# Optimization experiments

Measured on AMD Instinct MI355X. Metric: run time of the kernel, lower is better.

The kernel has to match this reference:

```python
import jax, jax.numpy as jnp
from jax import lax
import numpy as np

DN = ('NCHW', 'OIHW', 'NCHW')
PAD = [(1, 1), (1, 1)]  # padding=1 each side
STRIDE = (1, 1)


def setup_inputs() -> dict:
    key = jax.random.key(0)
    k0, k1, k2, k3, k4, k5 = jax.random.split(key, 6)
    B, Cin, Cout, H, W, K, FES = 32, 96, 144, 56, 56, 3, 3
    fan_main = Cin * K * K
    fan_extra = FES * K * K
    x = jax.random.normal(k0, (B, Cin, H, W), dtype=jnp.float32)
    extra_inputs = jax.random.normal(k1, (B, Cout * FES), dtype=jnp.float32)
    Wm = jax.random.normal(k2, (Cout, Cin, K, K), dtype=jnp.float32) / np.sqrt(fan_main)
    bm = jax.random.normal(k3, (Cout,), dtype=jnp.float32) * 0.01
    Wx = jax.random.normal(k4, (Cout, FES, K, K), dtype=jnp.float32) / np.sqrt(fan_extra)
    bx = jax.random.normal(k5, (Cout,), dtype=jnp.float32) * 0.01
    return {"x": x, "extra_inputs": extra_inputs, "Wm": Wm, "bm": bm, "Wx": Wx, "bx": bx}


def reference(x, extra_inputs, Wm, bm, Wx, bx):
    # main path: standard conv + bias
    main = lax.conv_general_dilated(x, Wm, STRIDE, PAD, dimension_numbers=DN)
    main = main + bm[None, :, None, None]

    B = x.shape[0]
    Cout, FES, kh, kw = Wx.shape
    H2, W2 = main.shape[2], main.shape[3]

    # Extra path: each extra conv operates on a spatially-constant map, so
    # conv(const_c) = const_c * conv(ones). Compute per-(out,fes)-kernel response
    # to a ones map once (captures zero-padding boundary effects exactly),
    # then combine via a batched einsum — collapsing the per-channel loop.
    ones = jnp.ones((1, 1, x.shape[2], x.shape[3]), dtype=x.dtype)
    M = lax.conv_general_dilated(
        ones, Wx.reshape(Cout * FES, 1, kh, kw), STRIDE, PAD, dimension_numbers=DN
    )  # [1, Cout*FES, H2, W2]
    M = M.reshape(Cout, FES, H2, W2)

    extra = extra_inputs.reshape(B, Cout, FES)
    extra_out = jnp.einsum('bif,ifhw->bihw', extra, M) + bx[None, :, None, None]

    return main + extra_out
```

## Files before the change

kernel.cpp:

```cpp
#include <hip/hip_runtime.h>
#include <hip/hip_bf16.h>

#define B_    32
#define CIN   96
#define COUT  144
#define H_    56
#define W_    56
#define HW    3136
#define NPIX  100352
#define KTOT  864
#define MT    128
#define TAPSZ (COUT*CIN)
#define W2    58
#define PLANE (W2*W2)
#define XTP_SHORTS ((size_t)B_ * PLANE * CIN)

typedef short  short8  __attribute__((ext_vector_type(8)));
typedef float  floatx4 __attribute__((ext_vector_type(4)));

__device__ __forceinline__ unsigned short f2bf(float f) {
    union { float f; unsigned int u; } v; v.f = f;
    unsigned int u = v.u;
    return (unsigned short)((u + 0x7FFFu + ((u >> 16) & 1u)) >> 16);
}

__device__ __forceinline__ void glds16(const void* g, void* l) {
    __builtin_amdgcn_global_load_lds(
        (const __attribute__((address_space(1))) unsigned int*)g,
        (__attribute__((address_space(3))) unsigned int*)l, 16, 0, 0);
}

#define TB 1568
#define WB 486
#define EB 18
#define ZB 342
__global__ __launch_bounds__(256) void prep_all(const float* __restrict__ x,
                                                unsigned short* __restrict__ xTp,
                                                const float* __restrict__ Wm,
                                                unsigned short* __restrict__ Wt,
                                                const float* __restrict__ extra,
                                                const float* __restrict__ Wx,
                                                const float* __restrict__ bm,
                                                const float* __restrict__ bx,
                                                float* __restrict__ E) {
    __shared__ __align__(16) unsigned short tile[64][CIN + 8];
    int blk = blockIdx.x;
    int t = threadIdx.x;
    if (blk < TB) {
        int b   = blk / 49;
        int hw0 = (blk % 49) * 64;
        const float* xb = x + (size_t)b * CIN * HW;
        for (int i = t; i < CIN * 16; i += 256) {
            int ci = i >> 4, seg = i & 15;
            float4 v = *(const float4*)(xb + (size_t)ci * HW + hw0 + seg * 4);
            int hwl = seg * 4;
            tile[hwl + 0][ci] = f2bf(v.x);
            tile[hwl + 1][ci] = f2bf(v.y);
            tile[hwl + 2][ci] = f2bf(v.z);
            tile[hwl + 3][ci] = f2bf(v.w);
        }
        __syncthreads();
        int row = t >> 2, part = t & 3;
        int hw = hw0 + row;
        int h  = hw / W_;
        int w  = hw - h * W_;
        const uint4* s = (const uint4*)&tile[row][part * 24];
        uint4* d = (uint4*)(xTp + ((size_t)((b * W2 + h + 1) * W2 + (w + 1))) * CIN
                                + part * 24);
        d[0] = s[0]; d[1] = s[1]; d[2] = s[2];
    } else if (blk < TB + WB) {
        int i = (blk - TB) * 256 + t;
        int tap = i / 13824;
        int r1  = i - tap * 13824;
        int g   = r1 / 1152;
        int r2  = r1 - g * 1152;
        int co  = r2 >> 3;
        int e   = r2 & 7;
        int ci  = g * 8 + e;
        Wt[i] = f2bf(Wm[((size_t)co * CIN + ci) * 9 + tap]);
    } else if (blk < TB + WB + EB) {
        int i = (blk - TB - WB) * 256 + t;
        int b = i / COUT, co = i - b * COUT;
        float base = bm[co] + bx[co];
        float m[3][3] = {{0,0,0},{0,0,0},{0,0,0}};
        for (int f = 0; f < 3; ++f) {
            float e = extra[(size_t)b * (COUT * 3) + co * 3 + f];
            const float* w = Wx + ((size_t)co * 3 + f) * 9;
            for (int rc = 0; rc < 3; ++rc) {
                int kh0 = (rc == 0) ? 1 : 0;
                int kh1 = (rc == 2) ? 1 : 2;
                for (int cc = 0; cc < 3; ++cc) {
                    int kw0 = (cc == 0) ? 1 : 0;
                    int kw1 = (cc == 2) ? 1 : 2;
                    float s = 0.f;
                    for (int kh = kh0; kh <= kh1; ++kh)
                        for (int kw = kw0; kw <= kw1; ++kw)
                            s += w[kh * 3 + kw];
                    m[rc][cc] += e * s;
                }
            }
        }
        float* dst = E + (size_t)i * 9;
        for (int rc = 0; rc < 3; ++rc)
            for (int cc = 0; cc < 3; ++cc)
                dst[rc * 3 + cc] = base + m[rc][cc];
    } else {
        int i = (blk - TB - WB - EB) * 256 + t;
        int b = i / 2736;
        int r = i - b * 2736;
        size_t base_b = (size_t)b * PLANE * CIN;
        size_t addr;
        if (r < 696) {
            addr = base_b + (size_t)r * 8;
        } else if (r < 1392) {
            addr = base_b + (size_t)57 * W2 * CIN + (size_t)(r - 696) * 8;
        } else if (r < 2064) {
            int r2 = r - 1392;
            int h = 1 + r2 / 12, u = r2 - (r2 / 12) * 12;
            addr = base_b + (size_t)(h * W2) * CIN + (size_t)u * 8;
        } else {
            int r2 = r - 2064;
            int h = 1 + r2 / 12, u = r2 - (r2 / 12) * 12;
            addr = base_b + (size_t)(h * W2 + 57) * CIN + (size_t)u * 8;
        }
        *(short8*)(xTp + addr) = (short8){0, 0, 0, 0, 0, 0, 0, 0};
    }
}

#define MFMA16(A, B, C) __builtin_amdgcn_mfma_f32_16x16x32_bf16(A, B, C, 0, 0, 0)

__global__ __launch_bounds__(256, 3) void conv_gemm(const unsigned short* __restrict__ xTp,
                                                    const unsigned short* __restrict__ Wt,
                                                    const float* __restrict__ E,
                                                    float* __restrict__ out) {
    __shared__ __align__(16) unsigned short Bs[TAPSZ];

    int tid = threadIdx.x;
    int wv = tid >> 6, lane = tid & 63;
    int r16 = lane & 15, q = lane >> 4;
    int pixBase = blockIdx.x * MT;

    floatx4 acc[2][9];
    #pragma unroll
    for (int m = 0; m < 2; ++m)
        #pragma unroll
        for (int n = 0; n < 9; ++n)
            acc[m][n] = (floatx4){0.f, 0.f, 0.f, 0.f};

    int aOff[2];
    #pragma unroll
    for (int ms = 0; ms < 2; ++ms) {
        int p = pixBase + wv * 32 + ms * 16 + r16;
        int b = p / HW;
        int hw = p - b * HW;
        int h = hw / W_;
        int w = hw - h * W_;
        aOff[ms] = ((b * W2 + h + 1) * W2 + (w + 1)) * CIN + q * 8;
    }

    const bool bTail = (tid < 192);

    const unsigned short* BpBase = Bs + (q * COUT + r16) * 8;

    short8 a[2][3];

    {
        const unsigned short* bT = xTp - (ptrdiff_t)((W2 + 1) * CIN);
        #pragma unroll
        for (int ms = 0; ms < 2; ++ms)
            #pragma unroll
            for (int ks = 0; ks < 3; ++ks)
                a[ms][ks] = *(const short8*)(bT + aOff[ms] + ks * 32);
    }

    #pragma unroll 1
    for (int tap = 0; tap < 9; ++tap) {
        const unsigned short* wsrc = Wt + tap * TAPSZ;
        #pragma unroll
        for (int j = 0; j < 6; ++j)
            glds16(wsrc + (tid + j * 256) * 8, (void*)(Bs + (tid + j * 256) * 8));
        if (bTail)
            glds16(wsrc + (1536 + tid) * 8, (void*)(Bs + (1536 + tid) * 8));
        __syncthreads();

        const int t1 = (tap < 8) ? tap + 1 : 8;
        const int r3 = (t1 * 11) >> 5;
        const unsigned short* bT =
            xTp + (ptrdiff_t)(((r3 - 1) * W2 + (t1 - r3 * 3 - 1)) * CIN);

        #pragma unroll
        for (int ks = 0; ks < 3; ++ks) {
            #pragma unroll
            for (int n3 = 0; n3 < 3; ++n3) {
                short8 b0 = *(const short8*)(BpBase + ks * 4608 + (n3 * 3 + 0) * 128);
                short8 b1 = *(const short8*)(BpBase + ks * 4608 + (n3 * 3 + 1) * 128);
                short8 b2 = *(const short8*)(BpBase + ks * 4608 + (n3 * 3 + 2) * 128);
                #pragma unroll
                for (int ms = 0; ms < 2; ++ms)
                    acc[ms][n3 * 3 + 0] = MFMA16(a[ms][ks], b0, acc[ms][n3 * 3 + 0]);
                #pragma unroll
                for (int ms = 0; ms < 2; ++ms)
                    acc[ms][n3 * 3 + 1] = MFMA16(a[ms][ks], b1, acc[ms][n3 * 3 + 1]);
                #pragma unroll
                for (int ms = 0; ms < 2; ++ms)
                    acc[ms][n3 * 3 + 2] = MFMA16(a[ms][ks], b2, acc[ms][n3 * 3 + 2]);
            }
            #pragma unroll
            for (int ms = 0; ms < 2; ++ms)
                a[ms][ks] = *(const short8*)(bT + aOff[ms] + ks * 32);
        }

        __syncthreads();
    }

    #pragma unroll
    for (int ms = 0; ms < 2; ++ms) {
        int p0 = pixBase + wv * 32 + ms * 16 + q * 4;
        int b  = p0 / HW;
        int hw0 = p0 - b * HW;
        int h = hw0 / W_;
        int w0 = hw0 - h * W_;
        int rc = (h == 0) ? 0 : ((h == H_ - 1) ? 2 : 1);
        int cc0 = (w0 == 0) ? 0 : ((w0 == W_ - 1) ? 2 : 1);
        int cc1 = (w0 + 1 == W_ - 1) ? 2 : 1;
        int cc2 = (w0 + 2 == W_ - 1) ? 2 : 1;
        int cc3 = (w0 + 3 == W_ - 1) ? 2 : 1;
        const float* Ebase = E + (size_t)b * COUT * 9 + rc * 3;
        float* outB = out + (size_t)b * COUT * HW + hw0;
        #pragma unroll
        for (int n = 0; n < 9; ++n) {
            int co = n * 16 + r16;
            const float* Eb = Ebase + co * 9;
            float4 v;
            v.x = acc[ms][n][0] + Eb[cc0];
            v.y = acc[ms][n][1] + Eb[cc1];
            v.z = acc[ms][n][2] + Eb[cc2];
            v.w = acc[ms][n][3] + Eb[cc3];
            *(float4*)(outB + (size_t)co * HW) = v;
        }
    }
}

extern "C" void kernel_launch(void* const* d_in, const int* in_sizes, int n_in,
                              void* d_out, int out_size, void* d_ws, size_t ws_size,
                              hipStream_t stream) {
    const float* x     = (const float*)d_in[0];
    const float* extra = (const float*)d_in[1];
    const float* Wm    = (const float*)d_in[2];
    const float* bm    = (const float*)d_in[3];
    const float* Wx    = (const float*)d_in[4];
    const float* bx    = (const float*)d_in[5];
    float* out = (float*)d_out;

    const size_t XT_BYTES = XTP_SHORTS * 2;
    const size_t WT_BYTES = (size_t)COUT * KTOT * 2;
    const size_t E_BYTES  = (size_t)B_ * COUT * 9 * 4;
    if (ws_size < XT_BYTES + WT_BYTES + E_BYTES) return;

    unsigned short* xTp = (unsigned short*)d_ws;
    unsigned short* Wt  = (unsigned short*)((char*)d_ws + XT_BYTES);
    float*          E   = (float*)((char*)d_ws + XT_BYTES + WT_BYTES);

    prep_all<<<TB + WB + EB + ZB, 256, 0, stream>>>(x, xTp, Wm, Wt, extra, Wx, bm, bx, E);
    conv_gemm<<<NPIX / MT, 256, 0, stream>>>(xTp, Wt, E, out);
}
```

Baseline: 150.1 us.

## Use single-wave blocks reading weights directly from global, dropping LDS staging

```diff
diff --git a/kernel.cpp b/kernel.cpp
--- a/kernel.cpp
+++ b/kernel.cpp
@@ -9,7 +9,7 @@
 #define HW    3136
 #define NPIX  100352
 #define KTOT  864
-#define MT    128
+#define MT    64
 #define TAPSZ (COUT*CIN)
 #define W2    58
 #define PLANE (W2*W2)
@@ -22,12 +22,6 @@
     union { float f; unsigned int u; } v; v.f = f;
     unsigned int u = v.u;
     return (unsigned short)((u + 0x7FFFu + ((u >> 16) & 1u)) >> 16);
-}
-
-__device__ __forceinline__ void glds16(const void* g, void* l) {
-    __builtin_amdgcn_global_load_lds(
-        (const __attribute__((address_space(1))) unsigned int*)g,
-        (__attribute__((address_space(3))) unsigned int*)l, 16, 0, 0);
 }
 
 #define TB 1568
@@ -129,28 +123,25 @@
 
 #define MFMA16(A, B, C) __builtin_amdgcn_mfma_f32_16x16x32_bf16(A, B, C, 0, 0, 0)
 
-__global__ __launch_bounds__(256, 3) void conv_gemm(const unsigned short* __restrict__ xTp,
-                                                    const unsigned short* __restrict__ Wt,
-                                                    const float* __restrict__ E,
-                                                    float* __restrict__ out) {
-    __shared__ __align__(16) unsigned short Bs[TAPSZ];
-
-    int tid = threadIdx.x;
-    int wv = tid >> 6, lane = tid & 63;
+__global__ __launch_bounds__(64, 2) void conv_gemm(const unsigned short* __restrict__ xTp,
+                                                   const unsigned short* __restrict__ Wt,
+                                                   const float* __restrict__ E,
+                                                   float* __restrict__ out) {
+    int lane = threadIdx.x;
     int r16 = lane & 15, q = lane >> 4;
     int pixBase = blockIdx.x * MT;
 
-    floatx4 acc[2][9];
+    floatx4 acc[4][9];
     #pragma unroll
-    for (int m = 0; m < 2; ++m)
+    for (int m = 0; m < 4; ++m)
         #pragma unroll
         for (int n = 0; n < 9; ++n)
             acc[m][n] = (floatx4){0.f, 0.f, 0.f, 0.f};
 
-    int aOff[2];
+    int aOff[4];
     #pragma unroll
-    for (int ms = 0; ms < 2; ++ms) {
-        int p = pixBase + wv * 32 + ms * 16 + r16;
+    for (int ms = 0; ms < 4; ++ms) {
+        int p = pixBase + ms * 16 + r16;
         int b = p / HW;
         int hw = p - b * HW;
         int h = hw / W_;
@@ -158,16 +149,14 @@
         aOff[ms] = ((b * W2 + h + 1) * W2 + (w + 1)) * CIN + q * 8;
     }
 
-    const bool bTail = (tid < 192);
-
-    const unsigned short* BpBase = Bs + (q * COUT + r16) * 8;
-
-    short8 a[2][3];
+    const unsigned short* Wb = Wt + q * 1152 + r16 * 8;
+
+    short8 a[4][3];
 
     {
         const unsigned short* bT = xTp - (ptrdiff_t)((W2 + 1) * CIN);
         #pragma unroll
-        for (int ms = 0; ms < 2; ++ms)
+        for (int ms = 0; ms < 4; ++ms)
             #pragma unroll
             for (int ks = 0; ks < 3; ++ks)
                 a[ms][ks] = *(const short8*)(bT + aOff[ms] + ks * 32);
@@ -175,13 +164,7 @@
 
     #pragma unroll 1
     for (int tap = 0; tap < 9; ++tap) {
-        const unsigned short* wsrc = Wt + tap * TAPSZ;
-        #pragma unroll
-        for (int j = 0; j < 6; ++j)
-            glds16(wsrc + (tid + j * 256) * 8, (void*)(Bs + (tid + j * 256) * 8));
-        if (bTail)
-            glds16(wsrc + (1536 + tid) * 8, (void*)(Bs + (1536 + tid) * 8));
-        __syncthreads();
+        const unsigned short* wtap = Wb + tap * TAPSZ;
 
         const int t1 = (tap < 8) ? tap + 1 : 8;
         const int r3 = (t1 * 11) >> 5;
@@ -192,30 +175,28 @@
         for (int ks = 0; ks < 3; ++ks) {
             #pragma unroll
             for (int n3 = 0; n3 < 3; ++n3) {
-                short8 b0 = *(const short8*)(BpBase + ks * 4608 + (n3 * 3 + 0) * 128);
-                short8 b1 = *(const short8*)(BpBase + ks * 4608 + (n3 * 3 + 1) * 128);
-                short8 b2 = *(const short8*)(BpBase + ks * 4608 + (n3 * 3 + 2) * 128);
+                short8 b0 = *(const short8*)(wtap + ks * 4608 + (n3 * 3 + 0) * 128);
+                short8 b1 = *(const short8*)(wtap + ks * 4608 + (n3 * 3 + 1) * 128);
+                short8 b2 = *(const short8*)(wtap + ks * 4608 + (n3 * 3 + 2) * 128);
                 #pragma unroll
-                for (int ms = 0; ms < 2; ++ms)
+                for (int ms = 0; ms < 4; ++ms)
                     acc[ms][n3 * 3 + 0] = MFMA16(a[ms][ks], b0, acc[ms][n3 * 3 + 0]);
                 #pragma unroll
-                for (int ms = 0; ms < 2; ++ms)
+                for (int ms = 0; ms < 4; ++ms)
                     acc[ms][n3 * 3 + 1] = MFMA16(a[ms][ks], b1, acc[ms][n3 * 3 + 1]);
                 #pragma unroll
-                for (int ms = 0; ms < 2; ++ms)
+                for (int ms = 0; ms < 4; ++ms)
                     acc[ms][n3 * 3 + 2] = MFMA16(a[ms][ks], b2, acc[ms][n3 * 3 + 2]);
             }
             #pragma unroll
-            for (int ms = 0; ms < 2; ++ms)
+            for (int ms = 0; ms < 4; ++ms)
                 a[ms][ks] = *(const short8*)(bT + aOff[ms] + ks * 32);
         }
-
-        __syncthreads();
     }
 
     #pragma unroll
-    for (int ms = 0; ms < 2; ++ms) {
-        int p0 = pixBase + wv * 32 + ms * 16 + q * 4;
+    for (int ms = 0; ms < 4; ++ms) {
+        int p0 = pixBase + ms * 16 + q * 4;
         int b  = p0 / HW;
         int hw0 = p0 - b * HW;
         int h = hw0 / W_;
@@ -262,5 +243,5 @@
     float*          E   = (float*)((char*)d_ws + XT_BYTES + WT_BYTES);
 
     prep_all<<<TB + WB + EB + ZB, 256, 0, stream>>>(x, xTp, Wm, Wt, extra, Wx, bm, bx, E);
-    conv_gemm<<<NPIX / MT, 256, 0, stream>>>(xTp, Wt, E, out);
-}
+    conv_gemm<<<NPIX / MT, 64, 0, stream>>>(xTp, Wt, E, out);
+}
```

New measurement: 160.7 us. 7.0% more time.

## Fuse prep and conv GEMM into one persistent kernel with grid barrier

Applied to the files above, without the earlier changes.

```diff
diff --git a/kernel.cpp b/kernel.cpp
--- a/kernel.cpp
+++ b/kernel.cpp
@@ -15,6 +15,14 @@
 #define PLANE (W2*W2)
 #define XTP_SHORTS ((size_t)B_ * PLANE * CIN)
 
+#define NBLK  768
+#define TB 1568
+#define WB 486
+#define EB 18
+#define ZB 342
+#define PREPB (TB + WB + EB + ZB)
+#define CONVB (NPIX / MT)
+
 typedef short  short8  __attribute__((ext_vector_type(8)));
 typedef float  floatx4 __attribute__((ext_vector_type(4)));
 
@@ -30,213 +38,215 @@
         (__attribute__((address_space(3))) unsigned int*)l, 16, 0, 0);
 }
 
-#define TB 1568
-#define WB 486
-#define EB 18
-#define ZB 342
-__global__ __launch_bounds__(256) void prep_all(const float* __restrict__ x,
-                                                unsigned short* __restrict__ xTp,
-                                                const float* __restrict__ Wm,
-                                                unsigned short* __restrict__ Wt,
-                                                const float* __restrict__ extra,
-                                                const float* __restrict__ Wx,
-                                                const float* __restrict__ bm,
-                                                const float* __restrict__ bx,
-                                                float* __restrict__ E) {
-    __shared__ __align__(16) unsigned short tile[64][CIN + 8];
-    int blk = blockIdx.x;
-    int t = threadIdx.x;
-    if (blk < TB) {
-        int b   = blk / 49;
-        int hw0 = (blk % 49) * 64;
-        const float* xb = x + (size_t)b * CIN * HW;
-        for (int i = t; i < CIN * 16; i += 256) {
-            int ci = i >> 4, seg = i & 15;
-            float4 v = *(const float4*)(xb + (size_t)ci * HW + hw0 + seg * 4);
-            int hwl = seg * 4;
-            tile[hwl + 0][ci] = f2bf(v.x);
-            tile[hwl + 1][ci] = f2bf(v.y);
-            tile[hwl + 2][ci] = f2bf(v.z);
-            tile[hwl + 3][ci] = f2bf(v.w);
+#define MFMA16(A, B, C) __builtin_amdgcn_mfma_f32_16x16x32_bf16(A, B, C, 0, 0, 0)
+
+__global__ __launch_bounds__(256, 3) void fused_all(
+    const float* __restrict__ x,  unsigned short* __restrict__ xTp,
+    const float* __restrict__ Wm, unsigned short* __restrict__ Wt,
+    const float* __restrict__ extra, const float* __restrict__ Wx,
+    const float* __restrict__ bm, const float* __restrict__ bx,
+    float* __restrict__ E, float* __restrict__ out,
+    unsigned int* __restrict__ bar)
+{
+    __shared__ __align__(16) unsigned char smem[TAPSZ * 2];
+    unsigned short (*tile)[CIN + 8] = (unsigned short (*)[CIN + 8])smem;
+    unsigned short *Bs = (unsigned short*)smem;
+
+    const int t = threadIdx.x;
+
+    for (int vb = blockIdx.x; vb < PREPB; vb += NBLK) {
+        if (vb < TB) {
+            int b   = vb / 49;
+            int hw0 = (vb % 49) * 64;
+            const float* xb = x + (size_t)b * CIN * HW;
+            for (int i = t; i < CIN * 16; i += 256) {
+                int ci  = (i & 15) + ((i >> 8) << 4);
+                int seg = (i >> 4) & 15;
+                float4 v = *(const float4*)(xb + (size_t)ci * HW + hw0 + seg * 4);
+                int hwl = seg * 4;
+                tile[hwl + 0][ci] = f2bf(v.x);
+                tile[hwl + 1][ci] = f2bf(v.y);
+                tile[hwl + 2][ci] = f2bf(v.z);
+                tile[hwl + 3][ci] = f2bf(v.w);
+            }
+            __syncthreads();
+            int row = t >> 2, part = t & 3;
+            int hw = hw0 + row;
+            int h  = hw / W_;
+            int w  = hw - h * W_;
+            const uint4* s = (const uint4*)&tile[row][part * 24];
+            uint4* d = (uint4*)(xTp + ((size_t)((b * W2 + h + 1) * W2 + (w + 1))) * CIN
+                                    + part * 24);
+            d[0] = s[0]; d[1] = s[1]; d[2] = s[2];
+        } else if (vb < TB + WB) {
+            int i = (vb - TB) * 256 + t;
+            int tap = i / 13824;
+            int r1  = i - tap * 13824;
+            int g   = r1 / 1152;
+            int r2  = r1 - g * 1152;
+            int co  = r2 >> 3;
+            int e   = r2 & 7;
+            int ci  = g * 8 + e;
+            Wt[i] = f2bf(Wm[((size_t)co * CIN + ci) * 9 + tap]);
+        } else if (vb < TB + WB + EB) {
+            int i = (vb - TB - WB) * 256 + t;
+            int b = i / COUT, co = i - b * COUT;
+            float base = bm[co] + bx[co];
+            float m[3][3] = {{0,0,0},{0,0,0},{0,0,0}};
+            for (int f = 0; f < 3; ++f) {
+                float e = extra[(size_t)b * (COUT * 3) + co * 3 + f];
+                const float* w = Wx + ((size_t)co * 3 + f) * 9;
+                for (int rc = 0; rc < 3; ++rc) {
+                    int kh0 = (rc == 0) ? 1 : 0;
+                    int kh1 = (rc == 2) ? 1 : 2;
+                    for (int cc = 0; cc < 3; ++cc) {
+                        int kw0 = (cc == 0) ? 1 : 0;
+                        int kw1 = (cc == 2) ? 1 : 2;
+                        float s = 0.f;
+                        for (int kh = kh0; kh <= kh1; ++kh)
+                            for (int kw = kw0; kw <= kw1; ++kw)
+                                s += w[kh * 3 + kw];
+                        m[rc][cc] += e * s;
+                    }
+                }
+            }
+            float* dst = E + (size_t)i * 9;
+            for (int rc = 0; rc < 3; ++rc)
+                for (int cc = 0; cc < 3; ++cc)
+                    dst[rc * 3 + cc] = base + m[rc][cc];
+        } else {
+            int i = (vb - TB - WB - EB) * 256 + t;
+            int b = i / 2736;
+            int r = i - b * 2736;
+            size_t base_b = (size_t)b * PLANE * CIN;
+            size_t addr;
+            if (r < 696) {
+                addr = base_b + (size_t)r * 8;
+            } else if (r < 1392) {
+                addr = base_b + (size_t)57 * W2 * CIN + (size_t)(r - 696) * 8;
+            } else if (r < 2064) {
+                int r2 = r - 1392;
+                int h = 1 + r2 / 12, u = r2 - (r2 / 12) * 12;
+                addr = base_b + (size_t)(h * W2) * CIN + (size_t)u * 8;
+            } else {
+                int r2 = r - 2064;
+                int h = 1 + r2 / 12, u = r2 - (r2 / 12) * 12;
+                addr = base_b + (size_t)(h * W2 + 57) * CIN + (size_t)u * 8;
+            }
+            *(short8*)(xTp + addr) = (short8){0, 0, 0, 0, 0, 0, 0, 0};
         }
         __syncthreads();
-        int row = t >> 2, part = t & 3;
-        int hw = hw0 + row;
-        int h  = hw / W_;
-        int w  = hw - h * W_;
-        const uint4* s = (const uint4*)&tile[row][part * 24];
-        uint4* d = (uint4*)(xTp + ((size_t)((b * W2 + h + 1) * W2 + (w + 1))) * CIN
-                                + part * 24);
-        d[0] = s[0]; d[1] = s[1]; d[2] = s[2];
-    } else if (blk < TB + WB) {
-        int i = (blk - TB) * 256 + t;
-        int tap = i / 13824;
-        int r1  = i - tap * 13824;
-        int g   = r1 / 1152;
-        int r2  = r1 - g * 1152;
-        int co  = r2 >> 3;
-        int e   = r2 & 7;
-        int ci  = g * 8 + e;
-        Wt[i] = f2bf(Wm[((size_t)co * CIN + ci) * 9 + tap]);
-    } else if (blk < TB + WB + EB) {
-        int i = (blk - TB - WB) * 256 + t;
-        int b = i / COUT, co = i - b * COUT;
-        float base = bm[co] + bx[co];
-        float m[3][3] = {{0,0,0},{0,0,0},{0,0,0}};
-        for (int f = 0; f < 3; ++f) {
-            float e = extra[(size_t)b * (COUT * 3) + co * 3 + f];
-            const float* w = Wx + ((size_t)co * 3 + f) * 9;
-            for (int rc = 0; rc < 3; ++rc) {
-                int kh0 = (rc == 0) ? 1 : 0;
-                int kh1 = (rc == 2) ? 1 : 2;
-                for (int cc = 0; cc < 3; ++cc) {
-                    int kw0 = (cc == 0) ? 1 : 0;
-                    int kw1 = (cc == 2) ? 1 : 2;
-                    float s = 0.f;
-                    for (int kh = kh0; kh <= kh1; ++kh)
-                        for (int kw = kw0; kw <= kw1; ++kw)
-                            s += w[kh * 3 + kw];
-                    m[rc][cc] += e * s;
+    }
+
+    __threadfence();
+    if (t == 0) {
+        __hip_atomic_fetch_add(bar, 1u, __ATOMIC_ACQ_REL, __HIP_MEMORY_SCOPE_AGENT);
+        while (__hip_atomic_load(bar, __ATOMIC_ACQUIRE, __HIP_MEMORY_SCOPE_AGENT) < NBLK)
+            __builtin_amdgcn_s_sleep(4);
+    }
+    __syncthreads();
+    __threadfence();
+
+    int wv = t >> 6, lane = t & 63;
+    int r16 = lane & 15, q = lane >> 4;
+    const bool bTail = (t < 192);
+    const unsigned short* BpBase = Bs + (q * COUT + r16) * 8;
+
+    for (int cb = blockIdx.x; cb < CONVB; cb += NBLK) {
+        int pixBase = cb * MT;
+
+        floatx4 acc[2][9];
+        #pragma unroll
+        for (int m = 0; m < 2; ++m)
+            #pragma unroll
+            for (int n = 0; n < 9; ++n)
+                acc[m][n] = (floatx4){0.f, 0.f, 0.f, 0.f};
+
+        int aOff[2];
+        #pragma unroll
+        for (int ms = 0; ms < 2; ++ms) {
+            int p = pixBase + wv * 32 + ms * 16 + r16;
+            int b = p / HW;
+            int hw = p - b * HW;
+            int h = hw / W_;
+            int w = hw - h * W_;
+            aOff[ms] = ((b * W2 + h + 1) * W2 + (w + 1)) * CIN + q * 8;
+        }
+
+        short8 a[2][3];
+        {
+            const unsigned short* bT = xTp - (ptrdiff_t)((W2 + 1) * CIN);
+            #pragma unroll
+            for (int ms = 0; ms < 2; ++ms)
+                #pragma unroll
+                for (int ks = 0; ks < 3; ++ks)
+                    a[ms][ks] = *(const short8*)(bT + aOff[ms] + ks * 32);
+        }
+
+        #pragma unroll 1
+        for (int tap = 0; tap < 9; ++tap) {
+            const unsigned short* wsrc = Wt + tap * TAPSZ;
+            #pragma unroll
+            for (int j = 0; j < 6; ++j)
+                glds16(wsrc + (t + j * 256) * 8, (void*)(Bs + (t + j * 256) * 8));
+            if (bTail)
+                glds16(wsrc + (1536 + t) * 8, (void*)(Bs + (1536 + t) * 8));
+            __syncthreads();
+
+            const int t1 = (tap < 8) ? tap + 1 : 8;
+            const int r3 = (t1 * 11) >> 5;
+            const unsigned short* bT =
+                xTp + (ptrdiff_t)(((r3 - 1) * W2 + (t1 - r3 * 3 - 1)) * CIN);
+
+            #pragma unroll
+            for (int ks = 0; ks < 3; ++ks) {
+                #pragma unroll
+                for (int n3 = 0; n3 < 3; ++n3) {
+                    short8 b0 = *(const short8*)(BpBase + ks * 4608 + (n3 * 3 + 0) * 128);
+                    short8 b1 = *(const short8*)(BpBase + ks * 4608 + (n3 * 3 + 1) * 128);
+                    short8 b2 = *(const short8*)(BpBase + ks * 4608 + (n3 * 3 + 2) * 128);
+                    #pragma unroll
+                    for (int ms = 0; ms < 2; ++ms)
+                        acc[ms][n3 * 3 + 0] = MFMA16(a[ms][ks], b0, acc[ms][n3 * 3 + 0]);
+                    #pragma unroll
+                    for (int ms = 0; ms < 2; ++ms)
+                        acc[ms][n3 * 3 + 1] = MFMA16(a[ms][ks], b1, acc[ms][n3 * 3 + 1]);
+                    #pragma unroll
+                    for (int ms = 0; ms < 2; ++ms)
+                        acc[ms][n3 * 3 + 2] = MFMA16(a[ms][ks], b2, acc[ms][n3 * 3 + 2]);
                 }
-            }
-        }
-        float* dst = E + (size_t)i * 9;
-        for (int rc = 0; rc < 3; ++rc)
-            for (int cc = 0; cc < 3; ++cc)
-                dst[rc * 3 + cc] = base + m[rc][cc];
-    } else {
-        int i = (blk - TB - WB - EB) * 256 + t;
-        int b = i / 2736;
-        int r = i - b * 2736;
-        size_t base_b = (size_t)b * PLANE * CIN;
-        size_t addr;
-        if (r < 696) {
-            addr = base_b + (size_t)r * 8;
-        } else if (r < 1392) {
-            addr = base_b + (size_t)57 * W2 * CIN + (size_t)(r - 696) * 8;
-        } else if (r < 2064) {
-            int r2 = r - 1392;
-            int h = 1 + r2 / 12, u = r2 - (r2 / 12) * 12;
-            addr = base_b + (size_t)(h * W2) * CIN + (size_t)u * 8;
-        } else {
-            int r2 = r - 2064;
-            int h = 1 + r2 / 12, u = r2 - (r2 / 12) * 12;
-            addr = base_b + (size_t)(h * W2 + 57) * CIN + (size_t)u * 8;
-        }
-        *(short8*)(xTp + addr) = (short8){0, 0, 0, 0, 0, 0, 0, 0};
-    }
-}
-
-#define MFMA16(A, B, C) __builtin_amdgcn_mfma_f32_16x16x32_bf16(A, B, C, 0, 0, 0)
-
-__global__ __launch_bounds__(256, 3) void conv_gemm(const unsigned short* __restrict__ xTp,
-                                                    const unsigned short* __restrict__ Wt,
-                                                    const float* __restrict__ E,
-                                                    float* __restrict__ out) {
-    __shared__ __align__(16) unsigned short Bs[TAPSZ];
-
-    int tid = threadIdx.x;
-    int wv = tid >> 6, lane = tid & 63;
-    int r16 = lane & 15, q = lane >> 4;
-    int pixBase = blockIdx.x * MT;
-
-    floatx4 acc[2][9];
-    #pragma unroll
-    for (int m = 0; m < 2; ++m)
-        #pragma unroll
-        for (int n = 0; n < 9; ++n)
-            acc[m][n] = (floatx4){0.f, 0.f, 0.f, 0.f};
-
-    int aOff[2];
-    #pragma unroll
-    for (int ms = 0; ms < 2; ++ms) {
-        int p = pixBase + wv * 32 + ms * 16 + r16;
-        int b = p / HW;
-        int hw = p - b * HW;
-        int h = hw / W_;
-        int w = hw - h * W_;
-        aOff[ms] = ((b * W2 + h + 1) * W2 + (w + 1)) * CIN + q * 8;
-    }
-
-    const bool bTail = (tid < 192);
-
-    const unsigned short* BpBase = Bs + (q * COUT + r16) * 8;
-
-    short8 a[2][3];
-
-    {
-        const unsigned short* bT = xTp - (ptrdiff_t)((W2 + 1) * CIN);
-        #pragma unroll
-        for (int ms = 0; ms < 2; ++ms)
-            #pragma unroll
-            for (int ks = 0; ks < 3; ++ks)
-                a[ms][ks] = *(const short8*)(bT + aOff[ms] + ks * 32);
-    }
-
-    #pragma unroll 1
-    for (int tap = 0; tap < 9; ++tap) {
-        const unsigned short* wsrc = Wt + tap * TAPSZ;
-        #pragma unroll
-        for (int j = 0; j < 6; ++j)
-            glds16(wsrc + (tid + j * 256) * 8, (void*)(Bs + (tid + j * 256) * 8));
-        if (bTail)
-            glds16(wsrc + (1536 + tid) * 8, (void*)(Bs + (1536 + tid) * 8));
-        __syncthreads();
-
-        const int t1 = (tap < 8) ? tap + 1 : 8;
-        const int r3 = (t1 * 11) >> 5;
-        const unsigned short* bT =
-            xTp + (ptrdiff_t)(((r3 - 1) * W2 + (t1 - r3 * 3 - 1)) * CIN);
-
-        #pragma unroll
-        for (int ks = 0; ks < 3; ++ks) {
-            #pragma unroll
-            for (int n3 = 0; n3 < 3; ++n3) {
-                short8 b0 = *(const short8*)(BpBase + ks * 4608 + (n3 * 3 + 0) * 128);
-                short8 b1 = *(const short8*)(BpBase + ks * 4608 + (n3 * 3 + 1) * 128);
-                short8 b2 = *(const short8*)(BpBase + ks * 4608 + (n3 * 3 + 2) * 128);
                 #pragma unroll
                 for (int ms = 0; ms < 2; ++ms)
-                    acc[ms][n3 * 3 + 0] = MFMA16(a[ms][ks], b0, acc[ms][n3 * 3 + 0]);
-                #pragma unroll
-                for (int ms = 0; ms < 2; ++ms)
-                    acc[ms][n3 * 3 + 1] = MFMA16(a[ms][ks], b1, acc[ms][n3 * 3 + 1]);
-                #pragma unroll
-                for (int ms = 0; ms < 2; ++ms)
-                    acc[ms][n3 * 3 + 2] = MFMA16(a[ms][ks], b2, acc[ms][n3 * 3 + 2]);
-            }
-            #pragma unroll
-            for (int ms = 0; ms < 2; ++ms)
-                a[ms][ks] = *(const short8*)(bT + aOff[ms] + ks * 32);
-        }
-
-        __syncthreads();
-    }
-
-    #pragma unroll
-    for (int ms = 0; ms < 2; ++ms) {
-        int p0 = pixBase + wv * 32 + ms * 16 + q * 4;
-        int b  = p0 / HW;
-        int hw0 = p0 - b * HW;
-        int h = hw0 / W_;
-        int w0 = hw0 - h * W_;
-        int rc = (h == 0) ? 0 : ((h == H_ - 1) ? 2 : 1);
-        int cc0 = (w0 == 0) ? 0 : ((w0 == W_ - 1) ? 2 : 1);
-        int cc1 = (w0 + 1 == W_ - 1) ? 2 : 1;
-        int cc2 = (w0 + 2 == W_ - 1) ? 2 : 1;
-        int cc3 = (w0 + 3 == W_ - 1) ? 2 : 1;
-        const float* Ebase = E + (size_t)b * COUT * 9 + rc * 3;
-        float* outB = out + (size_t)b * COUT * HW + hw0;
+                    a[ms][ks] = *(const short8*)(bT + aOff[ms] + ks * 32);
+            }
+            __syncthreads();
+        }
+
         #pragma unroll
-        for (int n = 0; n < 9; ++n) {
-            int co = n * 16 + r16;
-            const float* Eb = Ebase + co * 9;
-            float4 v;
-            v.x = acc[ms][n][0] + Eb[cc0];
-            v.y = acc[ms][n][1] + Eb[cc1];
-            v.z = acc[ms][n][2] + Eb[cc2];
-            v.w = acc[ms][n][3] + Eb[cc3];
-            *(float4*)(outB + (size_t)co * HW) = v;
+        for (int ms = 0; ms < 2; ++ms) {
+            int p0 = pixBase + wv * 32 + ms * 16 + q * 4;
+            int b  = p0 / HW;
+            int hw0 = p0 - b * HW;
+            int h = hw0 / W_;
+            int w0 = hw0 - h * W_;
+            int rc = (h == 0) ? 0 : ((h == H_ - 1) ? 2 : 1);
+            int cc0 = (w0 == 0) ? 0 : ((w0 == W_ - 1) ? 2 : 1);
+            int cc1 = (w0 + 1 == W_ - 1) ? 2 : 1;
+            int cc2 = (w0 + 2 == W_ - 1) ? 2 : 1;
+            int cc3 = (w0 + 3 == W_ - 1) ? 2 : 1;
+            const float* Ebase = E + (size_t)b * COUT * 9 + rc * 3;
+            float* outB = out + (size_t)b * COUT * HW + hw0;
+            #pragma unroll
+            for (int n = 0; n < 9; ++n) {
+                int co = n * 16 + r16;
+                const float* Eb = Ebase + co * 9;
+                float4 v;
+                v.x = acc[ms][n][0] + Eb[cc0];
+                v.y = acc[ms][n][1] + Eb[cc1];
+                v.z = acc[ms][n][2] + Eb[cc2];
+                v.w = acc[ms][n][3] + Eb[cc3];
+                *(float4*)(outB + (size_t)co * HW) = v;
+            }
         }
     }
 }
@@ -255,12 +265,14 @@
     const size_t XT_BYTES = XTP_SHORTS * 2;
     const size_t WT_BYTES = (size_t)COUT * KTOT * 2;
     const size_t E_BYTES  = (size_t)B_ * COUT * 9 * 4;
-    if (ws_size < XT_BYTES + WT_BYTES + E_BYTES) return;
+    const size_t BAR_OFF  = XT_BYTES + WT_BYTES + E_BYTES;
+    if (ws_size < BAR_OFF + 64) return;
 
     unsigned short* xTp = (unsigned short*)d_ws;
     unsigned short* Wt  = (unsigned short*)((char*)d_ws + XT_BYTES);
     float*          E   = (float*)((char*)d_ws + XT_BYTES + WT_BYTES);
-
-    prep_all<<<TB + WB + EB + ZB, 256, 0, stream>>>(x, xTp, Wm, Wt, extra, Wx, bm, bx, E);
-    conv_gemm<<<NPIX / MT, 256, 0, stream>>>(xTp, Wt, E, out);
-}
+    unsigned int*   bar = (unsigned int*)((char*)d_ws + BAR_OFF);
+
+    (void)hipMemsetAsync(bar, 0, 64, stream);
+    fused_all<<<NBLK, 256, 0, stream>>>(x, xTp, Wm, Wt, extra, Wx, bm, bx, E, out, bar);
+}
```

After: 371.6 us. 2.47x slower.
